# Optimization experiments

Measured on AMD Instinct MI355X. Metric: run time of the kernel, lower is better.

The kernel has to match this reference:

```python
import jax, jax.numpy as jnp
import numpy as np


def setup_inputs() -> dict:
    key = jax.random.key(0)
    ks = jax.random.split(key, 10)
    n_cells, n_genes, d, E = 10000, 2000, 128, 2000000
    return {
        "ufeats": jax.random.normal(ks[0], (n_cells, d), jnp.float32),
        "ifeats": jax.random.normal(ks[1], (n_genes, d), jnp.float32),
        "ge_factor": jax.random.uniform(ks[2], (n_genes, 1), jnp.float32),
        "sz_factor": jax.random.uniform(ks[3], (n_cells, 1), jnp.float32),
        "W_mean": jax.random.normal(ks[4], (d, 1), jnp.float32),
        "b_mean": jnp.zeros((1,), jnp.float32),
        "W_disp": jax.random.normal(ks[5], (d, 1), jnp.float32),
        "b_disp": jnp.zeros((1,), jnp.float32),
        "W_pi": jax.random.normal(ks[6], (d, 1), jnp.float32),
        "b_pi": jnp.zeros((1,), jnp.float32),
        "src_idx": jax.random.randint(ks[7], (E,), 0, n_cells, jnp.int64 if jax.config.read('jax_enable_x64') else jnp.int32),
        "dst_idx": jax.random.randint(ks[8], (E,), 0, n_genes, jnp.int64 if jax.config.read('jax_enable_x64') else jnp.int32),
    }


def reference(ufeats, ifeats, ge_factor, sz_factor,
              W_mean, b_mean, W_disp, b_disp, W_pi, b_pi,
              src_idx, dst_idx):
    # u_mul_v('h','h'): per-edge elementwise product of cell (u) and gene (v) feats -> [E, d]
    h_d = ufeats[src_idx] * ifeats[dst_idx]
    mu_ = jax.nn.sigmoid(h_d @ W_mean + b_mean)   # dec_mean: Linear + Sigmoid -> [E, 1]
    disp_ = h_d @ W_disp + b_disp                  # dec_disp: Linear -> [E, 1]
    pi = jax.nn.sigmoid(h_d @ W_pi + b_pi)         # dec_pi: Linear + Sigmoid -> [E, 1]
    gef = ge_factor[dst_idx]                       # u_mul_v('one','ge_factor') -> gene factor per edge
    szf = sz_factor[src_idx]                       # u_mul_v('sz_factor','one') -> cell size factor per edge
    disp = jnp.clip(jax.nn.softplus(gef * disp_), 1e-4, 1e4)          # DispAct
    mu = szf * jnp.clip(jnp.exp(gef * mu_) - 1.0, 1e-5, 1e6)          # MeanAct * sz_factor
    return (mu, disp, pi)
```

## Files before the change

### kernel.cpp

```cpp
#include <hip/hip_runtime.h>
#include <math.h>


typedef _Float16 h2 __attribute__((ext_vector_type(2)));
union U16 { uint4 u; h2 h[4]; };
union HU { uint u; h2 h; };

__global__ __launch_bounds__(256) void cvt_f16_fused_kernel(
    const float4* __restrict__ srcA, int nA4,
    const float4* __restrict__ srcB, int nB4,
    uint2* __restrict__ dst)
{
    int i = blockIdx.x * blockDim.x + threadIdx.x;
    if (i >= nA4 + nB4) return;
    float4 f = (i < nA4) ? srcA[i] : srcB[i - nA4];
    HU a, b;
    a.h = h2{(_Float16)f.x, (_Float16)f.y};
    b.h = h2{(_Float16)f.z, (_Float16)f.w};
    dst[i] = make_uint2(a.u, b.u);
}

__device__ __forceinline__ float reduce8t(
    float x0, float x1, float x2, float x3,
    float x4, float x5, float x6, float x7, int r)
{
    const bool h1 = (r & 1), h2b = (r & 2), h4 = (r & 4);
    float b0 = (h1 ? x1 : x0) + __shfl_xor(h1 ? x0 : x1, 1, 8);
    float b1 = (h1 ? x3 : x2) + __shfl_xor(h1 ? x2 : x3, 1, 8);
    float b2 = (h1 ? x5 : x4) + __shfl_xor(h1 ? x4 : x5, 1, 8);
    float b3 = (h1 ? x7 : x6) + __shfl_xor(h1 ? x6 : x7, 1, 8);
    float c0 = (h2b ? b1 : b0) + __shfl_xor(h2b ? b0 : b1, 2, 8);
    float c1 = (h2b ? b3 : b2) + __shfl_xor(h2b ? b2 : b3, 2, 8);
    return (h4 ? c1 : c0) + __shfl_xor(h4 ? c0 : c1, 4, 8);
}

__device__ __forceinline__ void dot3(
    const U16& ua, const U16& ub, const U16& va, const U16& vb,
    const h2* wm, const h2* wd, const h2* wp,
    float& m, float& dd, float& pp)
{
#pragma unroll
    for (int jj = 0; jj < 4; ++jj) {
        h2 p0 = ua.h[jj] * va.h[jj];
        m  = __builtin_amdgcn_fdot2(p0, wm[jj], m,  false);
        dd = __builtin_amdgcn_fdot2(p0, wd[jj], dd, false);
        pp = __builtin_amdgcn_fdot2(p0, wp[jj], pp, false);
        h2 p1 = ub.h[jj] * vb.h[jj];
        m  = __builtin_amdgcn_fdot2(p1, wm[4 + jj], m,  false);
        dd = __builtin_amdgcn_fdot2(p1, wd[4 + jj], dd, false);
        pp = __builtin_amdgcn_fdot2(p1, wp[4 + jj], pp, false);
    }
}

#define LOADE(J, SJ, GJ)                                                  \
    const uint4* uP##J = (const uint4*)(uhalf + (size_t)(SJ) * 128);      \
    const uint4* vP##J = (const uint4*)(ihalf + (size_t)(GJ) * 128);      \
    U16 uA##J, uB##J, vA##J, vB##J;                                       \
    uA##J.u = uP##J[r]; uB##J.u = uP##J[r + 8];                           \
    vA##J.u = vP##J[r]; vB##J.u = vP##J[r + 8];

__global__ __launch_bounds__(256, 2) void zinb_edge8_kernel(
    const _Float16* __restrict__ uhalf,
    const _Float16* __restrict__ ihalf,
    const float* __restrict__ ge_factor,
    const float* __restrict__ sz_factor,
    const float* __restrict__ W_mean, const float* __restrict__ b_mean,
    const float* __restrict__ W_disp, const float* __restrict__ b_disp,
    const float* __restrict__ W_pi,   const float* __restrict__ b_pi,
    const int* __restrict__ src_idx,
    const int* __restrict__ dst_idx,
    float* __restrict__ out,
    int E)
{
    const int tid = threadIdx.x;
    const int r = tid & 7;
    const int slot = (blockIdx.x * blockDim.x + tid) >> 3;
    const int n_slots = (gridDim.x * blockDim.x) >> 3;

    h2 wm[8], wd[8], wp[8];
#pragma unroll
    for (int c = 0; c < 2; ++c)
#pragma unroll
        for (int j = 0; j < 4; ++j) {
            int k = c * 64 + r * 8 + 2 * j;
            wm[c * 4 + j] = h2{(_Float16)W_mean[k], (_Float16)W_mean[k + 1]};
            wd[c * 4 + j] = h2{(_Float16)W_disp[k], (_Float16)W_disp[k + 1]};
            wp[c * 4 + j] = h2{(_Float16)W_pi[k],   (_Float16)W_pi[k + 1]};
        }
    const float bm = b_mean[0], bd = b_disp[0], bp = b_pi[0];

    const int nmac = E >> 3;
    const int4* src4 = (const int4*)src_idx;
    const int4* dst4 = (const int4*)dst_idx;

    for (int q = slot; q < nmac; q += n_slots) {
        const int e0 = q << 3;

        const int4 s03 = src4[2 * q];
        const int4 s47 = src4[2 * q + 1];
        const int4 g03 = dst4[2 * q];
        const int4 g47 = dst4[2 * q + 1];

        const int  se  = src_idx[e0 + r];
        const int  de  = dst_idx[e0 + r];
        const float szf = sz_factor[se];
        const float gef = ge_factor[de];

        LOADE(0, s03.x, g03.x)
        LOADE(1, s03.y, g03.y)
        LOADE(2, s03.z, g03.z)
        LOADE(3, s03.w, g03.w)
        LOADE(4, s47.x, g47.x)
        LOADE(5, s47.y, g47.y)
        LOADE(6, s47.z, g47.z)
        LOADE(7, s47.w, g47.w)

        float m0 = 0.f, d0 = 0.f, p0 = 0.f; dot3(uA0, uB0, vA0, vB0, wm, wd, wp, m0, d0, p0);
        float m1 = 0.f, d1 = 0.f, p1 = 0.f; dot3(uA1, uB1, vA1, vB1, wm, wd, wp, m1, d1, p1);
        float m2 = 0.f, d2 = 0.f, p2 = 0.f; dot3(uA2, uB2, vA2, vB2, wm, wd, wp, m2, d2, p2);
        float m3 = 0.f, d3 = 0.f, p3 = 0.f; dot3(uA3, uB3, vA3, vB3, wm, wd, wp, m3, d3, p3);
        float m4 = 0.f, d4 = 0.f, p4 = 0.f; dot3(uA4, uB4, vA4, vB4, wm, wd, wp, m4, d4, p4);
        float m5 = 0.f, d5 = 0.f, p5 = 0.f; dot3(uA5, uB5, vA5, vB5, wm, wd, wp, m5, d5, p5);
        float m6 = 0.f, d6 = 0.f, p6 = 0.f; dot3(uA6, uB6, vA6, vB6, wm, wd, wp, m6, d6, p6);
        float m7 = 0.f, d7 = 0.f, p7 = 0.f; dot3(uA7, uB7, vA7, vB7, wm, wd, wp, m7, d7, p7);

        const float rm = reduce8t(m0, m1, m2, m3, m4, m5, m6, m7, r);
        const float rd = reduce8t(d0, d1, d2, d3, d4, d5, d6, d7, r);
        const float rp = reduce8t(p0, p1, p2, p3, p4, p5, p6, p7, r);

        const float mu_ = 1.f / (1.f + __expf(-(rm + bm)));
        const float pi  = 1.f / (1.f + __expf(-(rp + bp)));
        const float xd  = gef * (rd + bd);
        const float sp  = fmaxf(xd, 0.f) + __logf(1.f + __expf(-fabsf(xd)));
        const float disp = fminf(fmaxf(sp, 1e-4f), 1e4f);
        const float mu = szf * fminf(fmaxf(__expf(gef * mu_) - 1.f, 1e-5f), 1e6f);

        const int e = e0 + r;
        out[e]                 = mu;
        out[(size_t)E + e]     = disp;
        out[(size_t)2 * E + e] = pi;
    }
}

__global__ void zinb_tail_kernel(
    const float* __restrict__ ufeats, const float* __restrict__ ifeats,
    const float* __restrict__ ge_factor, const float* __restrict__ sz_factor,
    const float* __restrict__ W_mean, const float* __restrict__ b_mean,
    const float* __restrict__ W_disp, const float* __restrict__ b_disp,
    const float* __restrict__ W_pi,   const float* __restrict__ b_pi,
    const int* __restrict__ src_idx, const int* __restrict__ dst_idx,
    float* __restrict__ out, int E, int start)
{
    int e = start + blockIdx.x * blockDim.x + threadIdx.x;
    if (e >= E) return;
    const int s = src_idx[e], g = dst_idx[e];
    float am = 0.f, ad = 0.f, ap = 0.f;
    for (int k = 0; k < 128; ++k) {
        float h = ufeats[(size_t)s * 128 + k] * ifeats[(size_t)g * 128 + k];
        am = fmaf(h, W_mean[k], am);
        ad = fmaf(h, W_disp[k], ad);
        ap = fmaf(h, W_pi[k],   ap);
    }
    const float gef = ge_factor[g];
    const float szf = sz_factor[s];
    const float mu_ = 1.f / (1.f + __expf(-(am + b_mean[0])));
    const float pi  = 1.f / (1.f + __expf(-(ap + b_pi[0])));
    const float xd  = gef * (ad + b_disp[0]);
    const float sp  = fmaxf(xd, 0.f) + __logf(1.f + __expf(-fabsf(xd)));
    const float disp = fminf(fmaxf(sp, 1e-4f), 1e4f);
    const float mu = szf * fminf(fmaxf(__expf(gef * mu_) - 1.f, 1e-5f), 1e6f);
    out[e] = mu; out[(size_t)E + e] = disp; out[(size_t)2 * E + e] = pi;
}

__global__ __launch_bounds__(256) void zinb_edge_f32_kernel(
    const float* __restrict__ ufeats, const float* __restrict__ ifeats,
    const float* __restrict__ ge_factor, const float* __restrict__ sz_factor,
    const float* __restrict__ W_mean, const float* __restrict__ b_mean,
    const float* __restrict__ W_disp, const float* __restrict__ b_disp,
    const float* __restrict__ W_pi,   const float* __restrict__ b_pi,
    const int* __restrict__ src_idx, const int* __restrict__ dst_idx,
    float* __restrict__ out, int E)
{
    const int r = threadIdx.x & 7;
    const int slot = (blockIdx.x * blockDim.x + threadIdx.x) >> 3;
    const int n_slots = (gridDim.x * blockDim.x) >> 3;

    float4 wm[4], wd[4], wp[4];
    {
        const float4* wm4 = (const float4*)W_mean + r;
        const float4* wd4 = (const float4*)W_disp + r;
        const float4* wp4 = (const float4*)W_pi   + r;
#pragma unroll
        for (int c = 0; c < 4; ++c) { wm[c] = wm4[c*8]; wd[c] = wd4[c*8]; wp[c] = wp4[c*8]; }
    }
    const float bm = b_mean[0], bd = b_disp[0], bp = b_pi[0];

    for (int e = slot; e < E; e += n_slots) {
        const int s = src_idx[e];
        const int g = dst_idx[e];
        const float4* u4 = (const float4*)(ufeats + (size_t)s * 128) + r;
        const float4* v4 = (const float4*)(ifeats + (size_t)g * 128) + r;
        float am = 0.f, ad = 0.f, ap = 0.f;
#pragma unroll
        for (int c = 0; c < 4; ++c) {
            float4 u = u4[c*8]; float4 v = v4[c*8];
            float px = u.x*v.x, py = u.y*v.y, pz = u.z*v.z, pw = u.w*v.w;
            am = fmaf(px, wm[c].x, am); am = fmaf(py, wm[c].y, am);
            am = fmaf(pz, wm[c].z, am); am = fmaf(pw, wm[c].w, am);
            ad = fmaf(px, wd[c].x, ad); ad = fmaf(py, wd[c].y, ad);
            ad = fmaf(pz, wd[c].z, ad); ad = fmaf(pw, wd[c].w, ad);
            ap = fmaf(px, wp[c].x, ap); ap = fmaf(py, wp[c].y, ap);
            ap = fmaf(pz, wp[c].z, ap); ap = fmaf(pw, wp[c].w, ap);
        }
#pragma unroll
        for (int off = 1; off < 8; off <<= 1) {
            am += __shfl_xor(am, off); ad += __shfl_xor(ad, off); ap += __shfl_xor(ap, off);
        }
        if (r == 0) {
            const float gef = ge_factor[g];
            const float szf = sz_factor[s];
            const float mu_ = 1.f / (1.f + __expf(-(am + bm)));
            const float pi  = 1.f / (1.f + __expf(-(ap + bp)));
            const float xd  = gef * (ad + bd);
            const float sp  = fmaxf(xd, 0.f) + __logf(1.f + __expf(-fabsf(xd)));
            const float disp = fminf(fmaxf(sp, 1e-4f), 1e4f);
            const float mu = szf * fminf(fmaxf(__expf(gef * mu_) - 1.f, 1e-5f), 1e6f);
            out[e] = mu; out[(size_t)E + e] = disp; out[(size_t)2*E + e] = pi;
        }
    }
}

extern "C" void kernel_launch(void* const* d_in, const int* in_sizes, int n_in,
                              void* d_out, int out_size, void* d_ws, size_t ws_size,
                              hipStream_t stream) {
    const float* ufeats    = (const float*)d_in[0];
    const float* ifeats    = (const float*)d_in[1];
    const float* ge_factor = (const float*)d_in[2];
    const float* sz_factor = (const float*)d_in[3];
    const float* W_mean    = (const float*)d_in[4];
    const float* b_mean    = (const float*)d_in[5];
    const float* W_disp    = (const float*)d_in[6];
    const float* b_disp    = (const float*)d_in[7];
    const float* W_pi      = (const float*)d_in[8];
    const float* b_pi      = (const float*)d_in[9];
    const int*   src_idx   = (const int*)d_in[10];
    const int*   dst_idx   = (const int*)d_in[11];
    float* out = (float*)d_out;

    const int E       = in_sizes[10];
    const int n_cells = in_sizes[0] / 128;
    const int n_genes = in_sizes[1] / 128;

    const size_t u_elems = (size_t)n_cells * 128;
    const size_t i_elems = (size_t)n_genes * 128;
    const size_t ws_needed = (u_elems + i_elems) * sizeof(_Float16);

    if (ws_size >= ws_needed) {
        _Float16* uhalf = (_Float16*)d_ws;
        _Float16* ihalf = uhalf + u_elems;

        const int un4 = (int)(u_elems / 4);
        const int in4 = (int)(i_elems / 4);
        const int n4  = un4 + in4;
        hipLaunchKernelGGL(cvt_f16_fused_kernel, dim3((n4 + 255) / 256), dim3(256), 0, stream,
                           (const float4*)ufeats, un4, (const float4*)ifeats, in4,
                           (uint2*)d_ws);

        hipLaunchKernelGGL(zinb_edge8_kernel, dim3(2048), dim3(256), 0, stream,
                           uhalf, ihalf, ge_factor, sz_factor,
                           W_mean, b_mean, W_disp, b_disp, W_pi, b_pi,
                           src_idx, dst_idx, out, E);

        const int rem = E & 7;
        if (rem) {
            hipLaunchKernelGGL(zinb_tail_kernel, dim3(1), dim3(64), 0, stream,
                               ufeats, ifeats, ge_factor, sz_factor,
                               W_mean, b_mean, W_disp, b_disp, W_pi, b_pi,
                               src_idx, dst_idx, out, E, E - rem);
        }
    } else {
        hipLaunchKernelGGL(zinb_edge_f32_kernel, dim3(2048), dim3(256), 0, stream,
                           ufeats, ifeats, ge_factor, sz_factor,
                           W_mean, b_mean, W_disp, b_disp, W_pi, b_pi,
                           src_idx, dst_idx, out, E);
    }
}
```

Baseline: 144.8 us.

## Restructure edge kernel to 16-lane groups with swizzled index broadcast and pipelined loads

The edge kernel moves from 8-lane to 16-lane groups, where each lane owns one 16-byte chunk of a 128-wide fp16 row. Edge indices are broadcast with ds_swizzle instead of redundant vector index loads. Gathers are double-buffered so the next edge's row loads issue while the current dot products run, and reductions are interleaved as pairwise xor folds. It also prefetches the next iteration's indices and raises the occupancy hint to 8 blocks per SM. This cuts register use and overlaps gather latency, at the cost of more shuffle traffic and serialised per-edge load chains.

Result: faster. 140.3 us (median of 2 runs) (-3.1%).

```diff
diff --git a/kernel.cpp b/kernel.cpp
--- a/kernel.cpp
+++ b/kernel.cpp
@@ -20,46 +20,37 @@
     dst[i] = make_uint2(a.u, b.u);
 }
 
-__device__ __forceinline__ float reduce8t(
-    float x0, float x1, float x2, float x3,
-    float x4, float x5, float x6, float x7, int r)
-{
-    const bool h1 = (r & 1), h2b = (r & 2), h4 = (r & 4);
-    float b0 = (h1 ? x1 : x0) + __shfl_xor(h1 ? x0 : x1, 1, 8);
-    float b1 = (h1 ? x3 : x2) + __shfl_xor(h1 ? x2 : x3, 1, 8);
-    float b2 = (h1 ? x5 : x4) + __shfl_xor(h1 ? x4 : x5, 1, 8);
-    float b3 = (h1 ? x7 : x6) + __shfl_xor(h1 ? x6 : x7, 1, 8);
-    float c0 = (h2b ? b1 : b0) + __shfl_xor(h2b ? b0 : b1, 2, 8);
-    float c1 = (h2b ? b3 : b2) + __shfl_xor(h2b ? b2 : b3, 2, 8);
-    return (h4 ? c1 : c0) + __shfl_xor(h4 ? c0 : c1, 4, 8);
-}
-
-__device__ __forceinline__ void dot3(
-    const U16& ua, const U16& ub, const U16& va, const U16& vb,
-    const h2* wm, const h2* wd, const h2* wp,
+__device__ __forceinline__ float foldx(float a, float b, int mask, int r)
+{
+    const bool hi = (r & mask) != 0;
+    const float keep = hi ? b : a;
+    const float send = hi ? a : b;
+    return keep + __shfl_xor(send, mask, 16);
+}
+
+__device__ __forceinline__ void dot16(
+    const U16& u, const U16& v,
+    const h2* __restrict__ wm, const h2* __restrict__ wd, const h2* __restrict__ wp,
     float& m, float& dd, float& pp)
 {
 #pragma unroll
     for (int jj = 0; jj < 4; ++jj) {
-        h2 p0 = ua.h[jj] * va.h[jj];
-        m  = __builtin_amdgcn_fdot2(p0, wm[jj], m,  false);
-        dd = __builtin_amdgcn_fdot2(p0, wd[jj], dd, false);
-        pp = __builtin_amdgcn_fdot2(p0, wp[jj], pp, false);
-        h2 p1 = ub.h[jj] * vb.h[jj];
-        m  = __builtin_amdgcn_fdot2(p1, wm[4 + jj], m,  false);
-        dd = __builtin_amdgcn_fdot2(p1, wd[4 + jj], dd, false);
-        pp = __builtin_amdgcn_fdot2(p1, wp[4 + jj], pp, false);
-    }
-}
-
-#define LOADE(J, SJ, GJ)                                                  \
-    const uint4* uP##J = (const uint4*)(uhalf + (size_t)(SJ) * 128);      \
-    const uint4* vP##J = (const uint4*)(ihalf + (size_t)(GJ) * 128);      \
-    U16 uA##J, uB##J, vA##J, vB##J;                                       \
-    uA##J.u = uP##J[r]; uB##J.u = uP##J[r + 8];                           \
-    vA##J.u = vP##J[r]; vB##J.u = vP##J[r + 8];
-
-__global__ __launch_bounds__(256, 2) void zinb_edge8_kernel(
+        h2 q = u.h[jj] * v.h[jj];
+        m  = __builtin_amdgcn_fdot2(q, wm[jj], m,  false);
+        dd = __builtin_amdgcn_fdot2(q, wd[jj], dd, false);
+        pp = __builtin_amdgcn_fdot2(q, wp[jj], pp, false);
+    }
+}
+
+#define SWZB(X, J) __builtin_amdgcn_ds_swizzle((X), 0x10 | ((J) << 5))
+
+#define PREF(J, U, V) {                                                   \
+    const int su_ = SWZB(se, J);                                          \
+    const int sg_ = SWZB(de, J);                                          \
+    (U).u = *((const uint4*)(uhalf + (size_t)su_ * 128) + r);             \
+    (V).u = *((const uint4*)(ihalf + (size_t)sg_ * 128) + r); }
+
+__global__ __launch_bounds__(256, 8) void zinb_edge16_kernel(
     const _Float16* __restrict__ uhalf,
     const _Float16* __restrict__ ihalf,
     const float* __restrict__ ge_factor,
@@ -73,64 +64,147 @@
     int E)
 {
     const int tid = threadIdx.x;
-    const int r = tid & 7;
-    const int slot = (blockIdx.x * blockDim.x + tid) >> 3;
-    const int n_slots = (gridDim.x * blockDim.x) >> 3;
-
-    h2 wm[8], wd[8], wp[8];
-#pragma unroll
-    for (int c = 0; c < 2; ++c)
-#pragma unroll
-        for (int j = 0; j < 4; ++j) {
-            int k = c * 64 + r * 8 + 2 * j;
-            wm[c * 4 + j] = h2{(_Float16)W_mean[k], (_Float16)W_mean[k + 1]};
-            wd[c * 4 + j] = h2{(_Float16)W_disp[k], (_Float16)W_disp[k + 1]};
-            wp[c * 4 + j] = h2{(_Float16)W_pi[k],   (_Float16)W_pi[k + 1]};
-        }
+    const int r = tid & 15;
+    const int slot = (blockIdx.x * blockDim.x + tid) >> 4;
+    const int n_slots = (gridDim.x * blockDim.x) >> 4;
+    const int nmac = E >> 4;
+
+    h2 wm[4], wd[4], wp[4];
+    {
+        const float4* a = (const float4*)W_mean + r * 2;
+        const float4* b = (const float4*)W_disp + r * 2;
+        const float4* c = (const float4*)W_pi   + r * 2;
+        float4 a0 = a[0], a1 = a[1];
+        float4 b0 = b[0], b1 = b[1];
+        float4 c0 = c[0], c1 = c[1];
+        wm[0] = h2{(_Float16)a0.x, (_Float16)a0.y}; wm[1] = h2{(_Float16)a0.z, (_Float16)a0.w};
+        wm[2] = h2{(_Float16)a1.x, (_Float16)a1.y}; wm[3] = h2{(_Float16)a1.z, (_Float16)a1.w};
+        wd[0] = h2{(_Float16)b0.x, (_Float16)b0.y}; wd[1] = h2{(_Float16)b0.z, (_Float16)b0.w};
+        wd[2] = h2{(_Float16)b1.x, (_Float16)b1.y}; wd[3] = h2{(_Float16)b1.z, (_Float16)b1.w};
+        wp[0] = h2{(_Float16)c0.x, (_Float16)c0.y}; wp[1] = h2{(_Float16)c0.z, (_Float16)c0.w};
+        wp[2] = h2{(_Float16)c1.x, (_Float16)c1.y}; wp[3] = h2{(_Float16)c1.z, (_Float16)c1.w};
+    }
     const float bm = b_mean[0], bd = b_disp[0], bp = b_pi[0];
 
-    const int nmac = E >> 3;
-    const int4* src4 = (const int4*)src_idx;
-    const int4* dst4 = (const int4*)dst_idx;
+    int se = 0, de = 0;
+    if (slot < nmac) {
+        se = src_idx[(slot << 4) + r];
+        de = dst_idx[(slot << 4) + r];
+    }
 
     for (int q = slot; q < nmac; q += n_slots) {
-        const int e0 = q << 3;
-
-        const int4 s03 = src4[2 * q];
-        const int4 s47 = src4[2 * q + 1];
-        const int4 g03 = dst4[2 * q];
-        const int4 g47 = dst4[2 * q + 1];
-
-        const int  se  = src_idx[e0 + r];
-        const int  de  = dst_idx[e0 + r];
+        const int e0 = q << 4;
         const float szf = sz_factor[se];
         const float gef = ge_factor[de];
 
-        LOADE(0, s03.x, g03.x)
-        LOADE(1, s03.y, g03.y)
-        LOADE(2, s03.z, g03.z)
-        LOADE(3, s03.w, g03.w)
-        LOADE(4, s47.x, g47.x)
-        LOADE(5, s47.y, g47.y)
-        LOADE(6, s47.z, g47.z)
-        LOADE(7, s47.w, g47.w)
-
-        float m0 = 0.f, d0 = 0.f, p0 = 0.f; dot3(uA0, uB0, vA0, vB0, wm, wd, wp, m0, d0, p0);
-        float m1 = 0.f, d1 = 0.f, p1 = 0.f; dot3(uA1, uB1, vA1, vB1, wm, wd, wp, m1, d1, p1);
-        float m2 = 0.f, d2 = 0.f, p2 = 0.f; dot3(uA2, uB2, vA2, vB2, wm, wd, wp, m2, d2, p2);
-        float m3 = 0.f, d3 = 0.f, p3 = 0.f; dot3(uA3, uB3, vA3, vB3, wm, wd, wp, m3, d3, p3);
-        float m4 = 0.f, d4 = 0.f, p4 = 0.f; dot3(uA4, uB4, vA4, vB4, wm, wd, wp, m4, d4, p4);
-        float m5 = 0.f, d5 = 0.f, p5 = 0.f; dot3(uA5, uB5, vA5, vB5, wm, wd, wp, m5, d5, p5);
-        float m6 = 0.f, d6 = 0.f, p6 = 0.f; dot3(uA6, uB6, vA6, vB6, wm, wd, wp, m6, d6, p6);
-        float m7 = 0.f, d7 = 0.f, p7 = 0.f; dot3(uA7, uB7, vA7, vB7, wm, wd, wp, m7, d7, p7);
-
-        const float rm = reduce8t(m0, m1, m2, m3, m4, m5, m6, m7, r);
-        const float rd = reduce8t(d0, d1, d2, d3, d4, d5, d6, d7, r);
-        const float rp = reduce8t(p0, p1, p2, p3, p4, p5, p6, p7, r);
-
-        const float mu_ = 1.f / (1.f + __expf(-(rm + bm)));
-        const float pi  = 1.f / (1.f + __expf(-(rp + bp)));
-        const float xd  = gef * (rd + bd);
+        U16 xu, xv, yu, yv;
+        PREF(0, xu, xv)
+        PREF(1, yu, yv)
+
+        const int qn = q + n_slots;
+        const int en0 = ((qn < nmac) ? qn : q) << 4;
+        const int se_n = src_idx[en0 + r];
+        const int de_n = dst_idx[en0 + r];
+
+        float Hm0, Hd0, Hp0;
+        {
+            float Am, Ad, Ap;
+            {
+                float m0 = 0.f, d0 = 0.f, p0 = 0.f;
+                dot16(xu, xv, wm, wd, wp, m0, d0, p0); PREF(2, xu, xv)
+                float m1 = 0.f, d1 = 0.f, p1 = 0.f;
+                dot16(yu, yv, wm, wd, wp, m1, d1, p1); PREF(3, yu, yv)
+                const float t0m = foldx(m0, m1, 1, r);
+                const float t0d = foldx(d0, d1, 1, r);
+                const float t0p = foldx(p0, p1, 1, r);
+                float m2 = 0.f, d2 = 0.f, p2 = 0.f;
+                dot16(xu, xv, wm, wd, wp, m2, d2, p2); PREF(4, xu, xv)
+                float m3 = 0.f, d3 = 0.f, p3 = 0.f;
+                dot16(yu, yv, wm, wd, wp, m3, d3, p3); PREF(5, yu, yv)
+                const float t1m = foldx(m2, m3, 1, r);
+                const float t1d = foldx(d2, d3, 1, r);
+                const float t1p = foldx(p2, p3, 1, r);
+                Am = foldx(t0m, t1m, 2, r);
+                Ad = foldx(t0d, t1d, 2, r);
+                Ap = foldx(t0p, t1p, 2, r);
+            }
+            float Bm, Bd, Bp;
+            {
+                float m0 = 0.f, d0 = 0.f, p0 = 0.f;
+                dot16(xu, xv, wm, wd, wp, m0, d0, p0); PREF(6, xu, xv)
+                float m1 = 0.f, d1 = 0.f, p1 = 0.f;
+                dot16(yu, yv, wm, wd, wp, m1, d1, p1); PREF(7, yu, yv)
+                const float t0m = foldx(m0, m1, 1, r);
+                const float t0d = foldx(d0, d1, 1, r);
+                const float t0p = foldx(p0, p1, 1, r);
+                float m2 = 0.f, d2 = 0.f, p2 = 0.f;
+                dot16(xu, xv, wm, wd, wp, m2, d2, p2); PREF(8, xu, xv)
+                float m3 = 0.f, d3 = 0.f, p3 = 0.f;
+                dot16(yu, yv, wm, wd, wp, m3, d3, p3); PREF(9, yu, yv)
+                const float t1m = foldx(m2, m3, 1, r);
+                const float t1d = foldx(d2, d3, 1, r);
+                const float t1p = foldx(p2, p3, 1, r);
+                Bm = foldx(t0m, t1m, 2, r);
+                Bd = foldx(t0d, t1d, 2, r);
+                Bp = foldx(t0p, t1p, 2, r);
+            }
+            Hm0 = foldx(Am, Bm, 4, r);
+            Hd0 = foldx(Ad, Bd, 4, r);
+            Hp0 = foldx(Ap, Bp, 4, r);
+        }
+        float Hm1, Hd1, Hp1;
+        {
+            float Cm, Cd, Cp;
+            {
+                float m0 = 0.f, d0 = 0.f, p0 = 0.f;
+                dot16(xu, xv, wm, wd, wp, m0, d0, p0); PREF(10, xu, xv)
+                float m1 = 0.f, d1 = 0.f, p1 = 0.f;
+                dot16(yu, yv, wm, wd, wp, m1, d1, p1); PREF(11, yu, yv)
+                const float t0m = foldx(m0, m1, 1, r);
+                const float t0d = foldx(d0, d1, 1, r);
+                const float t0p = foldx(p0, p1, 1, r);
+                float m2 = 0.f, d2 = 0.f, p2 = 0.f;
+                dot16(xu, xv, wm, wd, wp, m2, d2, p2); PREF(12, xu, xv)
+                float m3 = 0.f, d3 = 0.f, p3 = 0.f;
+                dot16(yu, yv, wm, wd, wp, m3, d3, p3); PREF(13, yu, yv)
+                const float t1m = foldx(m2, m3, 1, r);
+                const float t1d = foldx(d2, d3, 1, r);
+                const float t1p = foldx(p2, p3, 1, r);
+                Cm = foldx(t0m, t1m, 2, r);
+                Cd = foldx(t0d, t1d, 2, r);
+                Cp = foldx(t0p, t1p, 2, r);
+            }
+            float Dm, Dd, Dp;
+            {
+                float m0 = 0.f, d0 = 0.f, p0 = 0.f;
+                dot16(xu, xv, wm, wd, wp, m0, d0, p0); PREF(14, xu, xv)
+                float m1 = 0.f, d1 = 0.f, p1 = 0.f;
+                dot16(yu, yv, wm, wd, wp, m1, d1, p1); PREF(15, yu, yv)
+                const float t0m = foldx(m0, m1, 1, r);
+                const float t0d = foldx(d0, d1, 1, r);
+                const float t0p = foldx(p0, p1, 1, r);
+                float m2 = 0.f, d2 = 0.f, p2 = 0.f;
+                dot16(xu, xv, wm, wd, wp, m2, d2, p2);
+                float m3 = 0.f, d3 = 0.f, p3 = 0.f;
+                dot16(yu, yv, wm, wd, wp, m3, d3, p3);
+                const float t1m = foldx(m2, m3, 1, r);
+                const float t1d = foldx(d2, d3, 1, r);
+                const float t1p = foldx(p2, p3, 1, r);
+                Dm = foldx(t0m, t1m, 2, r);
+                Dd = foldx(t0d, t1d, 2, r);
+                Dp = foldx(t0p, t1p, 2, r);
+            }
+            Hm1 = foldx(Cm, Dm, 4, r);
+            Hd1 = foldx(Cd, Dd, 4, r);
+            Hp1 = foldx(Cp, Dp, 4, r);
+        }
+        const float Fm = foldx(Hm0, Hm1, 8, r);
+        const float Fd = foldx(Hd0, Hd1, 8, r);
+        const float Fp = foldx(Hp0, Hp1, 8, r);
+
+        const float mu_ = 1.f / (1.f + __expf(-(Fm + bm)));
+        const float pi  = 1.f / (1.f + __expf(-(Fp + bp)));
+        const float xd  = gef * (Fd + bd);
         const float sp  = fmaxf(xd, 0.f) + __logf(1.f + __expf(-fabsf(xd)));
         const float disp = fminf(fmaxf(sp, 1e-4f), 1e4f);
         const float mu = szf * fminf(fmaxf(__expf(gef * mu_) - 1.f, 1e-5f), 1e6f);
@@ -139,6 +213,8 @@
         out[e]                 = mu;
         out[(size_t)E + e]     = disp;
         out[(size_t)2 * E + e] = pi;
+
+        se = se_n; de = de_n;
     }
 }
 
@@ -266,12 +342,12 @@
                            (const float4*)ufeats, un4, (const float4*)ifeats, in4,
                            (uint2*)d_ws);
 
-        hipLaunchKernelGGL(zinb_edge8_kernel, dim3(2048), dim3(256), 0, stream,
+        hipLaunchKernelGGL(zinb_edge16_kernel, dim3(2048), dim3(256), 0, stream,
                            uhalf, ihalf, ge_factor, sz_factor,
                            W_mean, b_mean, W_disp, b_disp, W_pi, b_pi,
                            src_idx, dst_idx, out, E);
 
-        const int rem = E & 7;
+        const int rem = E & 15;
         if (rem) {
             hipLaunchKernelGGL(zinb_tail_kernel, dim3(1), dim3(64), 0, stream,
                                ufeats, ifeats, ge_factor, sz_factor,
```

## Compute per-edge decoder projections with MFMA and software-pipelined gathers

Applied to the files above, without the earlier changes.

Replaces the fdot2-based per-edge dot products and shuffle reductions with 16x16x32 f16 MFMA tiles. The three weight vectors are packed as B columns and 16 edges form the A rows. The loop software-pipelines the feature gathers and index loads one tile ahead, and each of three lanes writes a float4 per output. Occupancy hint raised to 4 blocks per CU. The kernel is likely memory-bound on gathers, so MFMA mainly removes VALU and shuffle overhead. Most of the 16 B columns are wasted, and only 3 of 16 lane columns do the epilogue, which risks divergence.

Result: slower. 231.1 us (+59.6%).

```diff
diff --git a/kernel.cpp b/kernel.cpp
--- a/kernel.cpp
+++ b/kernel.cpp
@@ -2,8 +2,10 @@
 #include <math.h>
 
 
+typedef _Float16 f16x8 __attribute__((ext_vector_type(8)));
+typedef float f32x4 __attribute__((ext_vector_type(4)));
 typedef _Float16 h2 __attribute__((ext_vector_type(2)));
-union U16 { uint4 u; h2 h[4]; };
+union U16 { uint4 u; f16x8 v; };
 union HU { uint u; h2 h; };
 
 __global__ __launch_bounds__(256) void cvt_f16_fused_kernel(
@@ -20,46 +22,7 @@
     dst[i] = make_uint2(a.u, b.u);
 }
 
-__device__ __forceinline__ float reduce8t(
-    float x0, float x1, float x2, float x3,
-    float x4, float x5, float x6, float x7, int r)
-{
-    const bool h1 = (r & 1), h2b = (r & 2), h4 = (r & 4);
-    float b0 = (h1 ? x1 : x0) + __shfl_xor(h1 ? x0 : x1, 1, 8);
-    float b1 = (h1 ? x3 : x2) + __shfl_xor(h1 ? x2 : x3, 1, 8);
-    float b2 = (h1 ? x5 : x4) + __shfl_xor(h1 ? x4 : x5, 1, 8);
-    float b3 = (h1 ? x7 : x6) + __shfl_xor(h1 ? x6 : x7, 1, 8);
-    float c0 = (h2b ? b1 : b0) + __shfl_xor(h2b ? b0 : b1, 2, 8);
-    float c1 = (h2b ? b3 : b2) + __shfl_xor(h2b ? b2 : b3, 2, 8);
-    return (h4 ? c1 : c0) + __shfl_xor(h4 ? c0 : c1, 4, 8);
-}
-
-__device__ __forceinline__ void dot3(
-    const U16& ua, const U16& ub, const U16& va, const U16& vb,
-    const h2* wm, const h2* wd, const h2* wp,
-    float& m, float& dd, float& pp)
-{
-#pragma unroll
-    for (int jj = 0; jj < 4; ++jj) {
-        h2 p0 = ua.h[jj] * va.h[jj];
-        m  = __builtin_amdgcn_fdot2(p0, wm[jj], m,  false);
-        dd = __builtin_amdgcn_fdot2(p0, wd[jj], dd, false);
-        pp = __builtin_amdgcn_fdot2(p0, wp[jj], pp, false);
-        h2 p1 = ub.h[jj] * vb.h[jj];
-        m  = __builtin_amdgcn_fdot2(p1, wm[4 + jj], m,  false);
-        dd = __builtin_amdgcn_fdot2(p1, wd[4 + jj], dd, false);
-        pp = __builtin_amdgcn_fdot2(p1, wp[4 + jj], pp, false);
-    }
-}
-
-#define LOADE(J, SJ, GJ)                                                  \
-    const uint4* uP##J = (const uint4*)(uhalf + (size_t)(SJ) * 128);      \
-    const uint4* vP##J = (const uint4*)(ihalf + (size_t)(GJ) * 128);      \
-    U16 uA##J, uB##J, vA##J, vB##J;                                       \
-    uA##J.u = uP##J[r]; uB##J.u = uP##J[r + 8];                           \
-    vA##J.u = vP##J[r]; vB##J.u = vP##J[r + 8];
-
-__global__ __launch_bounds__(256, 2) void zinb_edge8_kernel(
+__global__ __launch_bounds__(256, 4) void zinb_mfma_kernel(
     const _Float16* __restrict__ uhalf,
     const _Float16* __restrict__ ihalf,
     const float* __restrict__ ge_factor,
@@ -72,73 +35,125 @@
     float* __restrict__ out,
     int E)
 {
-    const int tid = threadIdx.x;
-    const int r = tid & 7;
-    const int slot = (blockIdx.x * blockDim.x + tid) >> 3;
-    const int n_slots = (gridDim.x * blockDim.x) >> 3;
-
-    h2 wm[8], wd[8], wp[8];
-#pragma unroll
-    for (int c = 0; c < 2; ++c)
-#pragma unroll
-        for (int j = 0; j < 4; ++j) {
-            int k = c * 64 + r * 8 + 2 * j;
-            wm[c * 4 + j] = h2{(_Float16)W_mean[k], (_Float16)W_mean[k + 1]};
-            wd[c * 4 + j] = h2{(_Float16)W_disp[k], (_Float16)W_disp[k + 1]};
-            wp[c * 4 + j] = h2{(_Float16)W_pi[k],   (_Float16)W_pi[k + 1]};
-        }
+    const int lane = threadIdx.x & 63;
+    const int col  = lane & 15;
+    const int kg   = lane >> 4;
+    const int w    = (blockIdx.x * blockDim.x + threadIdx.x) >> 6;
+    const int nw   = (gridDim.x * blockDim.x) >> 6;
+    const int ntiles = E >> 4;
+
+    const char* ubase = (const char*)uhalf;
+    const char* vbase = (const char*)ihalf;
+
+    f16x8 bfrag[4];
+    {
+        const float* Wsel = (col == 0) ? W_mean : (col == 1) ? W_disp : W_pi;
+#pragma unroll
+        for (int c = 0; c < 4; ++c) {
+            f16x8 b;
+#pragma unroll
+            for (int i = 0; i < 8; ++i) {
+                const float wv = Wsel[32 * c + 8 * kg + i];
+                b[i] = (col < 3) ? (_Float16)wv : (_Float16)0.f;
+            }
+            bfrag[c] = b;
+        }
+    }
     const float bm = b_mean[0], bd = b_disp[0], bp = b_pi[0];
 
-    const int nmac = E >> 3;
-    const int4* src4 = (const int4*)src_idx;
-    const int4* dst4 = (const int4*)dst_idx;
-
-    for (int q = slot; q < nmac; q += n_slots) {
-        const int e0 = q << 3;
-
-        const int4 s03 = src4[2 * q];
-        const int4 s47 = src4[2 * q + 1];
-        const int4 g03 = dst4[2 * q];
-        const int4 g47 = dst4[2 * q + 1];
-
-        const int  se  = src_idx[e0 + r];
-        const int  de  = dst_idx[e0 + r];
-        const float szf = sz_factor[se];
-        const float gef = ge_factor[de];
-
-        LOADE(0, s03.x, g03.x)
-        LOADE(1, s03.y, g03.y)
-        LOADE(2, s03.z, g03.z)
-        LOADE(3, s03.w, g03.w)
-        LOADE(4, s47.x, g47.x)
-        LOADE(5, s47.y, g47.y)
-        LOADE(6, s47.z, g47.z)
-        LOADE(7, s47.w, g47.w)
-
-        float m0 = 0.f, d0 = 0.f, p0 = 0.f; dot3(uA0, uB0, vA0, vB0, wm, wd, wp, m0, d0, p0);
-        float m1 = 0.f, d1 = 0.f, p1 = 0.f; dot3(uA1, uB1, vA1, vB1, wm, wd, wp, m1, d1, p1);
-        float m2 = 0.f, d2 = 0.f, p2 = 0.f; dot3(uA2, uB2, vA2, vB2, wm, wd, wp, m2, d2, p2);
-        float m3 = 0.f, d3 = 0.f, p3 = 0.f; dot3(uA3, uB3, vA3, vB3, wm, wd, wp, m3, d3, p3);
-        float m4 = 0.f, d4 = 0.f, p4 = 0.f; dot3(uA4, uB4, vA4, vB4, wm, wd, wp, m4, d4, p4);
-        float m5 = 0.f, d5 = 0.f, p5 = 0.f; dot3(uA5, uB5, vA5, vB5, wm, wd, wp, m5, d5, p5);
-        float m6 = 0.f, d6 = 0.f, p6 = 0.f; dot3(uA6, uB6, vA6, vB6, wm, wd, wp, m6, d6, p6);
-        float m7 = 0.f, d7 = 0.f, p7 = 0.f; dot3(uA7, uB7, vA7, vB7, wm, wd, wp, m7, d7, p7);
-
-        const float rm = reduce8t(m0, m1, m2, m3, m4, m5, m6, m7, r);
-        const float rd = reduce8t(d0, d1, d2, d3, d4, d5, d6, d7, r);
-        const float rp = reduce8t(p0, p1, p2, p3, p4, p5, p6, p7, r);
-
-        const float mu_ = 1.f / (1.f + __expf(-(rm + bm)));
-        const float pi  = 1.f / (1.f + __expf(-(rp + bp)));
-        const float xd  = gef * (rd + bd);
-        const float sp  = fmaxf(xd, 0.f) + __logf(1.f + __expf(-fabsf(xd)));
-        const float disp = fminf(fmaxf(sp, 1e-4f), 1e4f);
-        const float mu = szf * fminf(fmaxf(__expf(gef * mu_) - 1.f, 1e-5f), 1e6f);
-
-        const int e = e0 + r;
-        out[e]                 = mu;
-        out[(size_t)E + e]     = disp;
-        out[(size_t)2 * E + e] = pi;
+    int se_c = 0, de_c = 0, se_n = 0, de_n = 0;
+    U16 u0, u1, u2, u3, v0, v1, v2, v3;
+    if (w < ntiles) {
+        se_c = src_idx[(w << 4) + col];
+        de_c = dst_idx[(w << 4) + col];
+        const unsigned ou = (unsigned)se_c * 256u + ((unsigned)kg << 4);
+        const unsigned ov = (unsigned)de_c * 256u + ((unsigned)kg << 4);
+        u0.u = *(const uint4*)(ubase + ou);       u1.u = *(const uint4*)(ubase + ou + 64);
+        u2.u = *(const uint4*)(ubase + ou + 128); u3.u = *(const uint4*)(ubase + ou + 192);
+        v0.u = *(const uint4*)(vbase + ov);       v1.u = *(const uint4*)(vbase + ov + 64);
+        v2.u = *(const uint4*)(vbase + ov + 128); v3.u = *(const uint4*)(vbase + ov + 192);
+        int tn = w + nw; if (tn >= ntiles) tn = w;
+        se_n = src_idx[(tn << 4) + col];
+        de_n = dst_idx[(tn << 4) + col];
+    }
+
+    for (int t = w; t < ntiles; t += nw) {
+        const f16x8 a0 = u0.v * v0.v;
+        const f16x8 a1 = u1.v * v1.v;
+        const f16x8 a2 = u2.v * v2.v;
+        const f16x8 a3 = u3.v * v3.v;
+
+        {
+            const unsigned ou = (unsigned)se_n * 256u + ((unsigned)kg << 4);
+            const unsigned ov = (unsigned)de_n * 256u + ((unsigned)kg << 4);
+            u0.u = *(const uint4*)(ubase + ou);       u1.u = *(const uint4*)(ubase + ou + 64);
+            u2.u = *(const uint4*)(ubase + ou + 128); u3.u = *(const uint4*)(ubase + ou + 192);
+            v0.u = *(const uint4*)(vbase + ov);       v1.u = *(const uint4*)(vbase + ov + 64);
+            v2.u = *(const uint4*)(vbase + ov + 128); v3.u = *(const uint4*)(vbase + ov + 192);
+        }
+        int t2 = t + 2 * nw; if (t2 >= ntiles) t2 = t;
+        const int se_n2 = src_idx[(t2 << 4) + col];
+        const int de_n2 = dst_idx[(t2 << 4) + col];
+
+        f32x4 acc = {0.f, 0.f, 0.f, 0.f};
+        acc = __builtin_amdgcn_mfma_f32_16x16x32_f16(a0, bfrag[0], acc, 0, 0, 0);
+        acc = __builtin_amdgcn_mfma_f32_16x16x32_f16(a1, bfrag[1], acc, 0, 0, 0);
+        acc = __builtin_amdgcn_mfma_f32_16x16x32_f16(a2, bfrag[2], acc, 0, 0, 0);
+        acc = __builtin_amdgcn_mfma_f32_16x16x32_f16(a3, bfrag[3], acc, 0, 0, 0);
+
+        const int e0   = t << 4;
+        const int base = kg << 2;
+        const int s0 = __shfl(se_c, base + 0, 64);
+        const int s1 = __shfl(se_c, base + 1, 64);
+        const int s2 = __shfl(se_c, base + 2, 64);
+        const int s3 = __shfl(se_c, base + 3, 64);
+        const int g0 = __shfl(de_c, base + 0, 64);
+        const int g1 = __shfl(de_c, base + 1, 64);
+        const int g2 = __shfl(de_c, base + 2, 64);
+        const int g3 = __shfl(de_c, base + 3, 64);
+
+        if (col == 0) {
+            const float ge0 = ge_factor[g0], ge1 = ge_factor[g1],
+                        ge2 = ge_factor[g2], ge3 = ge_factor[g3];
+            const float sz0 = sz_factor[s0], sz1 = sz_factor[s1],
+                        sz2 = sz_factor[s2], sz3 = sz_factor[s3];
+            float4 o;
+            o.x = sz0 * fminf(fmaxf(__expf(ge0 / (1.f + __expf(-(acc[0] + bm)))) - 1.f, 1e-5f), 1e6f);
+            o.y = sz1 * fminf(fmaxf(__expf(ge1 / (1.f + __expf(-(acc[1] + bm)))) - 1.f, 1e-5f), 1e6f);
+            o.z = sz2 * fminf(fmaxf(__expf(ge2 / (1.f + __expf(-(acc[2] + bm)))) - 1.f, 1e-5f), 1e6f);
+            o.w = sz3 * fminf(fmaxf(__expf(ge3 / (1.f + __expf(-(acc[3] + bm)))) - 1.f, 1e-5f), 1e6f);
+            *(float4*)(out + e0 + base) = o;
+        } else if (col == 1) {
+            const float ge0 = ge_factor[g0], ge1 = ge_factor[g1],
+                        ge2 = ge_factor[g2], ge3 = ge_factor[g3];
+            float4 o;
+            {
+                const float xd = ge0 * (acc[0] + bd);
+                o.x = fminf(fmaxf(fmaxf(xd, 0.f) + __logf(1.f + __expf(-fabsf(xd))), 1e-4f), 1e4f);
+            }
+            {
+                const float xd = ge1 * (acc[1] + bd);
+                o.y = fminf(fmaxf(fmaxf(xd, 0.f) + __logf(1.f + __expf(-fabsf(xd))), 1e-4f), 1e4f);
+            }
+            {
+                const float xd = ge2 * (acc[2] + bd);
+                o.z = fminf(fmaxf(fmaxf(xd, 0.f) + __logf(1.f + __expf(-fabsf(xd))), 1e-4f), 1e4f);
+            }
+            {
+                const float xd = ge3 * (acc[3] + bd);
+                o.w = fminf(fmaxf(fmaxf(xd, 0.f) + __logf(1.f + __expf(-fabsf(xd))), 1e-4f), 1e4f);
+            }
+            *(float4*)(out + (size_t)E + e0 + base) = o;
+        } else if (col == 2) {
+            float4 o;
+            o.x = 1.f / (1.f + __expf(-(acc[0] + bp)));
+            o.y = 1.f / (1.f + __expf(-(acc[1] + bp)));
+            o.z = 1.f / (1.f + __expf(-(acc[2] + bp)));
+            o.w = 1.f / (1.f + __expf(-(acc[3] + bp)));
+            *(float4*)(out + (size_t)2 * E + e0 + base) = o;
+        }
+
+        se_c = se_n; de_c = de_n; se_n = se_n2; de_n = de_n2;
     }
 }
 
@@ -255,7 +270,7 @@
     const size_t i_elems = (size_t)n_genes * 128;
     const size_t ws_needed = (u_elems + i_elems) * sizeof(_Float16);
 
-    if (ws_size >= ws_needed) {
+    if (ws_size >= ws_needed && (E & 3) == 0) {
         _Float16* uhalf = (_Float16*)d_ws;
         _Float16* ihalf = uhalf + u_elems;
 
@@ -266,12 +281,12 @@
                            (const float4*)ufeats, un4, (const float4*)ifeats, in4,
                            (uint2*)d_ws);
 
-        hipLaunchKernelGGL(zinb_edge8_kernel, dim3(2048), dim3(256), 0, stream,
+        hipLaunchKernelGGL(zinb_mfma_kernel, dim3(2048), dim3(256), 0, stream,
                            uhalf, ihalf, ge_factor, sz_factor,
                            W_mean, b_mean, W_disp, b_disp, W_pi, b_pi,
                            src_idx, dst_idx, out, E);
 
-        const int rem = E & 7;
+        const int rem = E & 15;
         if (rem) {
             hipLaunchKernelGGL(zinb_tail_kernel, dim3(1), dim3(64), 0, stream,
                                ufeats, ifeats, ge_factor, sz_factor,
```
